# Optimization experiments

Measured on AMD Instinct MI355X. Metric: run time of the kernel, lower is better.

The kernel has to match this reference:

```python
import jax, jax.numpy as jnp
import numpy as np

USER_NUM = 100000
ITEM_NUM = 50000
EMBED_DIM = 64
N_LAYERS = 2
NNZ_UU, NNZ_UI, NNZ_II = 1600000, 2000000, 800000


def setup_inputs() -> dict:
    key = jax.random.key(0)
    ks = jax.random.split(key, 11)
    return {
        "user_embedding": jax.random.normal(ks[0], (USER_NUM, EMBED_DIM), jnp.float32),
        "item_embedding": jax.random.normal(ks[1], (ITEM_NUM, EMBED_DIM), jnp.float32),
        "uu_val": jax.random.uniform(ks[2], (NNZ_UU,), jnp.float32),
        "ui_val": jax.random.uniform(ks[3], (NNZ_UI,), jnp.float32),
        "ii_val": jax.random.uniform(ks[4], (NNZ_II,), jnp.float32),
        "uu_rows": jax.random.randint(ks[5], (NNZ_UU,), 0, USER_NUM, jnp.int32),
        "uu_cols": jax.random.randint(ks[6], (NNZ_UU,), 0, USER_NUM, jnp.int32),
        "ui_rows": jax.random.randint(ks[7], (NNZ_UI,), 0, USER_NUM, jnp.int32),
        "ui_cols": jax.random.randint(ks[8], (NNZ_UI,), 0, ITEM_NUM, jnp.int32),
        "ii_rows": jax.random.randint(ks[9], (NNZ_II,), 0, ITEM_NUM, jnp.int32),
        "ii_cols": jax.random.randint(ks[10], (NNZ_II,), 0, ITEM_NUM, jnp.int32),
    }


def _spmm(rows, cols, vals, x, n_out):
    # sparse(COO) @ dense: gather source features, scale by edge value, scatter-add to rows
    return jax.ops.segment_sum(vals[:, None] * x[cols], rows, num_segments=n_out)


def reference(user_embedding, item_embedding, uu_val, ui_val, ii_val,
              uu_rows, uu_cols, ui_rows, ui_cols, ii_rows, ii_cols):
    u = user_embedding
    i = item_embedding
    # running sum for mean over (n_layers + 1) layer outputs
    u_sum, i_sum = u, i
    for _ in range(N_LAYERS):
        u_from_i = _spmm(ui_rows, ui_cols, ui_val, i, USER_NUM)        # user_item_graph @ item
        i_from_u = _spmm(ui_cols, ui_rows, ui_val, u, ITEM_NUM)        # user_item_graph.T @ user
        uu = _spmm(uu_rows, uu_cols, uu_val, u, USER_NUM)              # user_graph @ user
        ii = _spmm(ii_rows, ii_cols, ii_val, i, ITEM_NUM)              # item_graph @ item
        u = 0.5 * (uu + u_from_i)   # mean over stacked pair
        i = 0.5 * (ii + i_from_u)
        u_sum = u_sum + u
        i_sum = i_sum + i
    inv = 1.0 / (N_LAYERS + 1)
    return u_sum * inv, i_sum * inv
```

## Files before the change

kernel.cpp:

```cpp
#include <hip/hip_runtime.h>

typedef _Float16 half8_t __attribute__((ext_vector_type(8)));
typedef _Float16 half4_t __attribute__((ext_vector_type(4)));

#define NU 100000
#define NI 50000
#define NR (NU + NI)
#define D 64
#define COARSE 1024
#define RPB 147
#define CAP 8800
#define CHUNK 6144
#define RPT 6
#define NT4 (NR * 16)
#define PKSLACK 448

__global__ void init_kernel(const float4* __restrict__ ue, const float4* __restrict__ ie,
                            float4* __restrict__ out, half4_t* __restrict__ curh) {
    int idx = blockIdx.x * 256 + threadIdx.x;
    if (idx >= NT4) return;
    float4 v = (idx < NU * 16) ? ue[idx] : ie[idx - NU * 16];
    out[idx] = v;
    half4_t h;
    h[0] = (_Float16)v.x; h[1] = (_Float16)v.y; h[2] = (_Float16)v.z; h[3] = (_Float16)v.w;
    curh[idx] = h;
}

__device__ __forceinline__ int place_dest(int p, const int* ui_r, const int* ui_c,
                                          const int* uu_r, const int* ii_r,
                                          int n_ui, int n_uu) {
    if (p < 2 * n_ui) {
        int e = p >> 1;
        return (p & 1) ? NU + ui_c[e] : ui_r[e];
    } else if (p < 2 * n_ui + n_uu) {
        return uu_r[p - 2 * n_ui];
    } else {
        return NU + ii_r[p - 2 * n_ui - n_uu];
    }
}

__global__ void count_kernel(const int* __restrict__ ui_r, const int* __restrict__ ui_c,
                             const int* __restrict__ uu_r, const int* __restrict__ ii_r,
                             int* __restrict__ m, int n_ui, int n_uu, int nnzt) {
    __shared__ int cnt[COARSE];
    int tid = threadIdx.x;
    cnt[tid] = 0;
    __syncthreads();
    int blk0 = blockIdx.x * CHUNK;
#pragma unroll
    for (int k = 0; k < RPT; k++) {
        int p = blk0 + k * 1024 + tid;
        if (p < nnzt) {
            int dest = place_dest(p, ui_r, ui_c, uu_r, ii_r, n_ui, n_uu);
            atomicAdd(&cnt[dest / RPB], 1);
        }
    }
    __syncthreads();
    m[blockIdx.x * COARSE + tid] = cnt[tid];
}

__global__ void colsum_kernel(const int* __restrict__ m, int* __restrict__ tots, int nblk) {
    __shared__ int s[256];
    int c = blockIdx.x, tid = threadIdx.x;
    int sum = 0;
    for (int b = tid; b < nblk; b += 256) sum += m[b * COARSE + c];
    s[tid] = sum;
    __syncthreads();
    for (int off = 128; off > 0; off >>= 1) {
        if (tid < off) s[tid] += s[tid + off];
        __syncthreads();
    }
    if (tid == 0) tots[c] = s[0];
}

__global__ void scan1_kernel(const int* __restrict__ tots, int* __restrict__ coarse_base) {
    __shared__ int s[COARSE];
    int tid = threadIdx.x;
    int x = tots[tid];
    s[tid] = x;
    __syncthreads();
    for (int off = 1; off < COARSE; off <<= 1) {
        int t = (tid >= off) ? s[tid - off] : 0;
        __syncthreads();
        s[tid] += t;
        __syncthreads();
    }
    coarse_base[tid] = s[tid] - x;
    if (tid == COARSE - 1) coarse_base[COARSE] = s[tid];
}

__global__ void rebase_kernel(int* __restrict__ m, const int* __restrict__ coarse_base, int nblk) {
    __shared__ int s[256];
    int c = blockIdx.x, tid = threadIdx.x;
    int K = (nblk + 255) / 256;
    int b0 = tid * K;
    int b1 = b0 + K;
    if (b1 > nblk) b1 = nblk;
    int sum = 0;
    for (int b = b0; b < b1; b++) sum += m[b * COARSE + c];
    s[tid] = sum;
    __syncthreads();
    for (int off = 1; off < 256; off <<= 1) {
        int t = (tid >= off) ? s[tid - off] : 0;
        __syncthreads();
        s[tid] += t;
        __syncthreads();
    }
    int run = coarse_base[c] + s[tid] - sum;
    for (int b = b0; b < b1; b++) {
        int v = m[b * COARSE + c];
        m[b * COARSE + c] = run;
        run += v;
    }
}

__global__ void place_kernel(const int* __restrict__ ui_r, const int* __restrict__ ui_c,
                             const float* __restrict__ ui_v,
                             const int* __restrict__ uu_r, const int* __restrict__ uu_c,
                             const float* __restrict__ uu_v,
                             const int* __restrict__ ii_r, const int* __restrict__ ii_c,
                             const float* __restrict__ ii_v,
                             const int* __restrict__ m, uint2* __restrict__ scratch,
                             int n_ui, int n_uu, int nnzt) {
    __shared__ uint2 rec[CHUNK];
    __shared__ int cnt[COARSE];
    __shared__ int lbase[COARSE];
    __shared__ int base_s[COARSE];
    __shared__ int s_ntot;
    int tid = threadIdx.x;
    cnt[tid] = 0;
    __syncthreads();
    int blk0 = blockIdx.x * CHUNK;
    int rk[RPT];
#pragma unroll
    for (int k = 0; k < RPT; k++) {
        int p = blk0 + k * 1024 + tid;
        rk[k] = -1;
        if (p < nnzt) {
            int dest = place_dest(p, ui_r, ui_c, uu_r, ii_r, n_ui, n_uu);
            int c = dest / RPB;
            int lr = atomicAdd(&cnt[c], 1);
            rk[k] = (c << 14) | lr;
        }
    }
    __syncthreads();
    int own = cnt[tid];
    lbase[tid] = own;
    __syncthreads();
    for (int off = 1; off < COARSE; off <<= 1) {
        int t = (tid >= off) ? lbase[tid - off] : 0;
        __syncthreads();
        lbase[tid] += t;
        __syncthreads();
    }
    int incl = lbase[tid];
    __syncthreads();
    lbase[tid] = incl - own;
    if (tid == COARSE - 1) s_ntot = incl;
    base_s[tid] = m[blockIdx.x * COARSE + tid];
    __syncthreads();
#pragma unroll
    for (int k = 0; k < RPT; k++) {
        int p = blk0 + k * 1024 + tid;
        if (p >= nnzt) continue;
        int dest, src;
        float v;
        if (p < 2 * n_ui) {
            int e = p >> 1;
            int r = ui_r[e], cc = ui_c[e];
            v = ui_v[e];
            if (p & 1) { dest = NU + cc; src = r; }
            else       { dest = r; src = NU + cc; }
        } else if (p < 2 * n_ui + n_uu) {
            int e = p - 2 * n_ui;
            dest = uu_r[e]; src = uu_c[e]; v = uu_v[e];
        } else {
            int e = p - 2 * n_ui - n_uu;
            dest = NU + ii_r[e]; src = NU + ii_c[e]; v = ii_v[e];
        }
        int c  = rk[k] >> 14;
        int lr = rk[k] & 0x3FFF;
        int dl = dest - c * RPB;
        _Float16 hv = (_Float16)v;
        unsigned short us;
        __builtin_memcpy(&us, &hv, 2);
        rec[lbase[c] + lr] = make_uint2(((unsigned)dl << 18) | (unsigned)src,
                                        ((unsigned)c << 16) | (unsigned)us);
    }
    __syncthreads();
    int ntot = s_ntot;
    for (int i = tid; i < ntot; i += 1024) {
        uint2 r = rec[i];
        int c = r.y >> 16;
        scratch[base_s[c] + (i - lbase[c])] = r;
    }
}

__global__ void csr_kernel(const uint2* __restrict__ scratch, const int* __restrict__ coarse_base,
                           int* __restrict__ ptr, int* __restrict__ pk_src,
                           unsigned short* __restrict__ pk_val) {
    __shared__ int s[1024];
    __shared__ int fine[256];
    __shared__ int fill[256];
    __shared__ int lsrc[CAP];
    __shared__ unsigned short lval[CAP];
    __shared__ int s_pn;
    int c = blockIdx.x, tid = threadIdx.x;
    int rbeg = c * RPB;
    int rcnt = NR - rbeg;
    if (rcnt > RPB) rcnt = RPB;
    if (rcnt < 0) rcnt = 0;
    int base = coarse_base[c], end = coarse_base[c + 1];
    int n = end - base;
    int pkc    = ((base + 3) & ~3) + c * PKSLACK;
    int pknext = ((end  + 3) & ~3) + (c + 1) * PKSLACK;
    if (tid < 256) fine[tid] = 0;
    __syncthreads();
    for (int i = tid; i < n; i += 1024)
        atomicAdd(&fine[scratch[base + i].x >> 18], 1);
    __syncthreads();
    int own = (tid < 256) ? fine[tid] : 0;
    int own4 = (own + 3) & ~3;
    s[tid] = own4;
    __syncthreads();
    for (int off = 1; off < 256; off <<= 1) {
        int t = (tid >= off) ? s[tid - off] : 0;
        __syncthreads();
        s[tid] += t;
        __syncthreads();
    }
    int excl4 = s[tid] - own4;
    if (tid < rcnt) ptr[rbeg + tid] = pkc + excl4;
    if (tid == 0 && rbeg + rcnt == NR) ptr[NR] = pknext;
    if (tid < 256) fill[tid] = excl4;
    if (tid == 255) s_pn = s[255];
    __syncthreads();
    int pn = s_pn;
    if (pn <= CAP) {
        for (int i = tid; i < pn; i += 1024) { lsrc[i] = 0; lval[i] = 0; }
        __syncthreads();
        for (int i = tid; i < n; i += 1024) {
            uint2 rec = scratch[base + i];
            int dl = rec.x >> 18;
            int slot = atomicAdd(&fill[dl], 1);
            lsrc[slot] = rec.x & 0x3FFFF;
            lval[slot] = (unsigned short)rec.y;
        }
        __syncthreads();
        for (int i = tid; i < pn; i += 1024) {
            pk_src[pkc + i] = lsrc[i] << 7;
            pk_val[pkc + i] = lval[i];
        }
        for (int i = pkc + pn + tid; i < pknext; i += 1024) { pk_src[i] = 0; pk_val[i] = 0; }
    } else {
        for (int i = pkc + tid; i < pknext; i += 1024) { pk_src[i] = 0; pk_val[i] = 0; }
        __syncthreads();
        for (int i = tid; i < n; i += 1024) {
            uint2 rec = scratch[base + i];
            int dl = rec.x >> 18;
            int slot = atomicAdd(&fill[dl], 1);
            pk_src[pkc + slot] = (rec.x & 0x3FFFF) << 7;
            pk_val[pkc + slot] = (unsigned short)rec.y;
        }
    }
}

__global__ void spmm_fused(const int* __restrict__ ptr, const int* __restrict__ pk_src,
                           const half4_t* __restrict__ pk_val4,
                           const half8_t* __restrict__ src,
                           half8_t* __restrict__ nexth, float4* __restrict__ out,
                           float final_scale, int store_next) {
    int w = (int)((blockIdx.x * blockDim.x + threadIdx.x) >> 6);
    int lane = threadIdx.x & 63;
    if (w >= NR) return;
    int g = lane >> 3;
    int fl = lane & 7;
    const char* sph = (const char*)src + (fl << 4);
    const int4* ps = (const int4*)pk_src;

    int b = ptr[w], e = ptr[w + 1];
    int q0 = b >> 2, qe = e >> 2;

    float acc[8];
#pragma unroll
    for (int k = 0; k < 8; k++) acc[k] = 0.f;

    for (int q = q0 + g; q < qe; q += 8) {
        int4 sa = ps[q];
        half4_t va = pk_val4[q];
        half8_t x0 = *(const half8_t*)(sph + sa.x);
        half8_t x1 = *(const half8_t*)(sph + sa.y);
        half8_t x2 = *(const half8_t*)(sph + sa.z);
        half8_t x3 = *(const half8_t*)(sph + sa.w);
        float v0 = (float)va[0];
        float v1 = (float)va[1];
        float v2 = (float)va[2];
        float v3 = (float)va[3];
#pragma unroll
        for (int k = 0; k < 8; k++) {
            acc[k] += v0 * (float)x0[k];
            acc[k] += v1 * (float)x1[k];
            acc[k] += v2 * (float)x2[k];
            acc[k] += v3 * (float)x3[k];
        }
    }

#pragma unroll
    for (int k = 0; k < 8; k++) {
        acc[k] += __shfl_xor(acc[k], 8);
        acc[k] += __shfl_xor(acc[k], 16);
        acc[k] += __shfl_xor(acc[k], 32);
    }

    if (lane < 8) {
        float h[8];
#pragma unroll
        for (int k = 0; k < 8; k++) h[k] = 0.5f * acc[k];
        if (store_next) {
            half8_t hh;
#pragma unroll
            for (int k = 0; k < 8; k++) hh[k] = (_Float16)h[k];
            nexth[w * 8 + lane] = hh;
        }
        float4* op = out + (size_t)w * 16 + lane * 2;
        float4 o0 = op[0];
        float4 o1 = op[1];
        o0.x = (o0.x + h[0]) * final_scale;
        o0.y = (o0.y + h[1]) * final_scale;
        o0.z = (o0.z + h[2]) * final_scale;
        o0.w = (o0.w + h[3]) * final_scale;
        o1.x = (o1.x + h[4]) * final_scale;
        o1.y = (o1.y + h[5]) * final_scale;
        o1.z = (o1.z + h[6]) * final_scale;
        o1.w = (o1.w + h[7]) * final_scale;
        op[0] = o0;
        op[1] = o1;
    }
}

extern "C" void kernel_launch(void* const* d_in, const int* in_sizes, int n_in,
                              void* d_out, int out_size, void* d_ws, size_t ws_size,
                              hipStream_t stream) {
    const float* ue      = (const float*)d_in[0];
    const float* ie      = (const float*)d_in[1];
    const float* uu_val  = (const float*)d_in[2];
    const float* ui_val  = (const float*)d_in[3];
    const float* ii_val  = (const float*)d_in[4];
    const int*   uu_rows = (const int*)d_in[5];
    const int*   uu_cols = (const int*)d_in[6];
    const int*   ui_rows = (const int*)d_in[7];
    const int*   ui_cols = (const int*)d_in[8];
    const int*   ii_rows = (const int*)d_in[9];
    const int*   ii_cols = (const int*)d_in[10];

    const int NNZ_UU = in_sizes[2];
    const int NNZ_UI = in_sizes[3];
    const int NNZ_II = in_sizes[4];
    const int NNZT   = 2 * NNZ_UI + NNZ_UU + NNZ_II;
    const int NBLK   = (NNZT + CHUNK - 1) / CHUNK;
    const int PKTOT  = NNZT + PKSLACK * COARSE + 64;

    float* out = (float*)d_out;

    char* wsb = (char*)d_ws;
    half8_t* curh   = (half8_t*)wsb;
    uint2*   scratch = (uint2*)(wsb + (size_t)NR * 128);
    half8_t* nexth  = (half8_t*)scratch;
    int*     pk_src = (int*)(scratch + NNZT);
    unsigned short* pk_val = (unsigned short*)(pk_src + PKTOT);
    int*     ptr    = (int*)(pk_val + PKTOT);
    int*     coarse_base = ptr + (NR + 1);
    int*     tots   = coarse_base + (COARSE + 1);
    int*     m      = tots + COARSE;

    init_kernel<<<(NT4 + 255) / 256, 256, 0, stream>>>(
        (const float4*)ue, (const float4*)ie, (float4*)out, (half4_t*)curh);

    count_kernel<<<NBLK, 1024, 0, stream>>>(
        ui_rows, ui_cols, uu_rows, ii_rows, m, NNZ_UI, NNZ_UU, NNZT);

    colsum_kernel<<<COARSE, 256, 0, stream>>>(m, tots, NBLK);
    scan1_kernel<<<1, 1024, 0, stream>>>(tots, coarse_base);
    rebase_kernel<<<COARSE, 256, 0, stream>>>(m, coarse_base, NBLK);

    place_kernel<<<NBLK, 1024, 0, stream>>>(
        ui_rows, ui_cols, ui_val, uu_rows, uu_cols, uu_val,
        ii_rows, ii_cols, ii_val, m, scratch, NNZ_UI, NNZ_UU, NNZT);

    csr_kernel<<<COARSE, 1024, 0, stream>>>(scratch, coarse_base, ptr, pk_src, pk_val);

    int blocks = (NR * 64 + 511) / 512;

    spmm_fused<<<blocks, 512, 0, stream>>>(
        ptr, pk_src, (const half4_t*)pk_val, curh, nexth, (float4*)out, 1.0f, 1);

    spmm_fused<<<blocks, 512, 0, stream>>>(
        ptr, pk_src, (const half4_t*)pk_val, nexth, curh, (float4*)out, 1.0f / 3.0f, 0);
}
```

Measured before the change: 491.7 us.

## Process four rows per wavefront in SpMM with two edge-groups per row

Changes the SpMM work mapping so that each 64-lane wavefront handles four output rows, each served by 16 lanes split into two edge groups, where before a whole wave handled one row with eight groups. The cross-lane reduction shrinks to a single shuffle, and the half-precision store and fp32 output update are split across the two halves. The aim is to cut idle lanes and reduction overhead, since the average row has about 29 edges (roughly 7 packed quads). In exchange, each lane runs a longer serial loop with less memory parallelism per row, and rows of different lengths within one wave can diverge.

```diff
diff --git a/kernel.cpp b/kernel.cpp
--- a/kernel.cpp
+++ b/kernel.cpp
@@ -270,22 +270,24 @@
                            const half8_t* __restrict__ src,
                            half8_t* __restrict__ nexth, float4* __restrict__ out,
                            float final_scale, int store_next) {
-    int w = (int)((blockIdx.x * blockDim.x + threadIdx.x) >> 6);
+    int wave = (int)((blockIdx.x * blockDim.x + threadIdx.x) >> 6);
     int lane = threadIdx.x & 63;
-    if (w >= NR) return;
-    int g = lane >> 3;
+    int sl = lane >> 4;
+    int h  = (lane >> 3) & 1;
     int fl = lane & 7;
+    int row = wave * 4 + sl;
+    if (row >= NR) return;
     const char* sph = (const char*)src + (fl << 4);
     const int4* ps = (const int4*)pk_src;
 
-    int b = ptr[w], e = ptr[w + 1];
+    int b = ptr[row], e = ptr[row + 1];
     int q0 = b >> 2, qe = e >> 2;
 
     float acc[8];
 #pragma unroll
     for (int k = 0; k < 8; k++) acc[k] = 0.f;
 
-    for (int q = q0 + g; q < qe; q += 8) {
+    for (int q = q0 + h; q < qe; q += 2) {
         int4 sa = ps[q];
         half4_t va = pk_val4[q];
         half8_t x0 = *(const half8_t*)(sph + sa.x);
@@ -306,33 +308,31 @@
     }
 
 #pragma unroll
-    for (int k = 0; k < 8; k++) {
-        acc[k] += __shfl_xor(acc[k], 8);
-        acc[k] += __shfl_xor(acc[k], 16);
-        acc[k] += __shfl_xor(acc[k], 32);
-    }
-
-    if (lane < 8) {
-        float h[8];
-#pragma unroll
-        for (int k = 0; k < 8; k++) h[k] = 0.5f * acc[k];
+    for (int k = 0; k < 8; k++) acc[k] += __shfl_xor(acc[k], 8);
+
+    float hv[8];
+#pragma unroll
+    for (int k = 0; k < 8; k++) hv[k] = 0.5f * acc[k];
+
+    if (h == 0) {
         if (store_next) {
             half8_t hh;
 #pragma unroll
-            for (int k = 0; k < 8; k++) hh[k] = (_Float16)h[k];
-            nexth[w * 8 + lane] = hh;
-        }
-        float4* op = out + (size_t)w * 16 + lane * 2;
+            for (int k = 0; k < 8; k++) hh[k] = (_Float16)hv[k];
+            nexth[row * 8 + fl] = hh;
+        }
+    } else {
+        float4* op = out + (size_t)row * 16 + fl * 2;
         float4 o0 = op[0];
         float4 o1 = op[1];
-        o0.x = (o0.x + h[0]) * final_scale;
-        o0.y = (o0.y + h[1]) * final_scale;
-        o0.z = (o0.z + h[2]) * final_scale;
-        o0.w = (o0.w + h[3]) * final_scale;
-        o1.x = (o1.x + h[4]) * final_scale;
-        o1.y = (o1.y + h[5]) * final_scale;
-        o1.z = (o1.z + h[6]) * final_scale;
-        o1.w = (o1.w + h[7]) * final_scale;
+        o0.x = (o0.x + hv[0]) * final_scale;
+        o0.y = (o0.y + hv[1]) * final_scale;
+        o0.z = (o0.z + hv[2]) * final_scale;
+        o0.w = (o0.w + hv[3]) * final_scale;
+        o1.x = (o1.x + hv[4]) * final_scale;
+        o1.y = (o1.y + hv[5]) * final_scale;
+        o1.z = (o1.z + hv[6]) * final_scale;
+        o1.w = (o1.w + hv[7]) * final_scale;
         op[0] = o0;
         op[1] = o1;
     }
@@ -389,7 +389,8 @@
 
     csr_kernel<<<COARSE, 1024, 0, stream>>>(scratch, coarse_base, ptr, pk_src, pk_val);
 
-    int blocks = (NR * 64 + 511) / 512;
+    int waves = (NR + 3) / 4;
+    int blocks = (waves * 64 + 511) / 512;
 
     spmm_fused<<<blocks, 512, 0, stream>>>(
         ptr, pk_src, (const half4_t*)pk_val, curh, nexth, (float4*)out, 1.0f, 1);
```

Result: slower. 507.4 us (+3.2%).

## Replace per-block count matrix with global atomics; drop colsum and rebase kernels

Applied to the files above, without the earlier changes.

Count blocks now atomically add their bucket counts into a global totals array, and place blocks claim output ranges with atomicAdd on a per-bucket cursor. This removes the colsum and rebase kernel launches and the per-block count matrix traffic. The place kernel keeps each edge's source and value in registers so it does not reload the inputs. The csr kernel caches scratch records in registers, and init no longer writes the float output: layer 0 writes it directly and layer 1 adds the original embeddings. Record order within a bucket becomes nondeterministic, which can change float summation order between runs.

```diff
diff --git a/kernel.cpp b/kernel.cpp
--- a/kernel.cpp
+++ b/kernel.cpp
@@ -12,15 +12,16 @@
 #define CAP 8800
 #define CHUNK 6144
 #define RPT 6
+#define RPT2 9
 #define NT4 (NR * 16)
 #define PKSLACK 448
 
 __global__ void init_kernel(const float4* __restrict__ ue, const float4* __restrict__ ie,
-                            float4* __restrict__ out, half4_t* __restrict__ curh) {
+                            half4_t* __restrict__ curh, int* __restrict__ tots) {
     int idx = blockIdx.x * 256 + threadIdx.x;
+    if (idx < COARSE) tots[idx] = 0;
     if (idx >= NT4) return;
     float4 v = (idx < NU * 16) ? ue[idx] : ie[idx - NU * 16];
-    out[idx] = v;
     half4_t h;
     h[0] = (_Float16)v.x; h[1] = (_Float16)v.y; h[2] = (_Float16)v.z; h[3] = (_Float16)v.w;
     curh[idx] = h;
@@ -41,7 +42,7 @@
 
 __global__ void count_kernel(const int* __restrict__ ui_r, const int* __restrict__ ui_c,
                              const int* __restrict__ uu_r, const int* __restrict__ ii_r,
-                             int* __restrict__ m, int n_ui, int n_uu, int nnzt) {
+                             int* __restrict__ tots, int n_ui, int n_uu, int nnzt) {
     __shared__ int cnt[COARSE];
     int tid = threadIdx.x;
     cnt[tid] = 0;
@@ -56,24 +57,11 @@
         }
     }
     __syncthreads();
-    m[blockIdx.x * COARSE + tid] = cnt[tid];
-}
-
-__global__ void colsum_kernel(const int* __restrict__ m, int* __restrict__ tots, int nblk) {
-    __shared__ int s[256];
-    int c = blockIdx.x, tid = threadIdx.x;
-    int sum = 0;
-    for (int b = tid; b < nblk; b += 256) sum += m[b * COARSE + c];
-    s[tid] = sum;
-    __syncthreads();
-    for (int off = 128; off > 0; off >>= 1) {
-        if (tid < off) s[tid] += s[tid + off];
-        __syncthreads();
-    }
-    if (tid == 0) tots[c] = s[0];
-}
-
-__global__ void scan1_kernel(const int* __restrict__ tots, int* __restrict__ coarse_base) {
+    if (cnt[tid]) atomicAdd(&tots[tid], cnt[tid]);
+}
+
+__global__ void scan1_kernel(const int* __restrict__ tots, int* __restrict__ coarse_base,
+                             int* __restrict__ cursor) {
     __shared__ int s[COARSE];
     int tid = threadIdx.x;
     int x = tots[tid];
@@ -85,33 +73,10 @@
         s[tid] += t;
         __syncthreads();
     }
-    coarse_base[tid] = s[tid] - x;
+    int excl = s[tid] - x;
+    coarse_base[tid] = excl;
+    cursor[tid] = excl;
     if (tid == COARSE - 1) coarse_base[COARSE] = s[tid];
-}
-
-__global__ void rebase_kernel(int* __restrict__ m, const int* __restrict__ coarse_base, int nblk) {
-    __shared__ int s[256];
-    int c = blockIdx.x, tid = threadIdx.x;
-    int K = (nblk + 255) / 256;
-    int b0 = tid * K;
-    int b1 = b0 + K;
-    if (b1 > nblk) b1 = nblk;
-    int sum = 0;
-    for (int b = b0; b < b1; b++) sum += m[b * COARSE + c];
-    s[tid] = sum;
-    __syncthreads();
-    for (int off = 1; off < 256; off <<= 1) {
-        int t = (tid >= off) ? s[tid - off] : 0;
-        __syncthreads();
-        s[tid] += t;
-        __syncthreads();
-    }
-    int run = coarse_base[c] + s[tid] - sum;
-    for (int b = b0; b < b1; b++) {
-        int v = m[b * COARSE + c];
-        m[b * COARSE + c] = run;
-        run += v;
-    }
 }
 
 __global__ void place_kernel(const int* __restrict__ ui_r, const int* __restrict__ ui_c,
@@ -120,7 +85,7 @@
                              const float* __restrict__ uu_v,
                              const int* __restrict__ ii_r, const int* __restrict__ ii_c,
                              const float* __restrict__ ii_v,
-                             const int* __restrict__ m, uint2* __restrict__ scratch,
+                             int* __restrict__ cursor, uint2* __restrict__ scratch,
                              int n_ui, int n_uu, int nnzt) {
     __shared__ uint2 rec[CHUNK];
     __shared__ int cnt[COARSE];
@@ -131,20 +96,41 @@
     cnt[tid] = 0;
     __syncthreads();
     int blk0 = blockIdx.x * CHUNK;
-    int rk[RPT];
+    unsigned rk[RPT];
+    int sk[RPT];
+    unsigned short vk[RPT];
 #pragma unroll
     for (int k = 0; k < RPT; k++) {
         int p = blk0 + k * 1024 + tid;
-        rk[k] = -1;
+        rk[k] = 0xFFFFFFFFu;
         if (p < nnzt) {
-            int dest = place_dest(p, ui_r, ui_c, uu_r, ii_r, n_ui, n_uu);
+            int dest, src;
+            float v;
+            if (p < 2 * n_ui) {
+                int e = p >> 1;
+                int r = ui_r[e], cc = ui_c[e];
+                v = ui_v[e];
+                if (p & 1) { dest = NU + cc; src = r; }
+                else       { dest = r; src = NU + cc; }
+            } else if (p < 2 * n_ui + n_uu) {
+                int e = p - 2 * n_ui;
+                dest = uu_r[e]; src = uu_c[e]; v = uu_v[e];
+            } else {
+                int e = p - 2 * n_ui - n_uu;
+                dest = NU + ii_r[e]; src = NU + ii_c[e]; v = ii_v[e];
+            }
             int c = dest / RPB;
             int lr = atomicAdd(&cnt[c], 1);
-            rk[k] = (c << 14) | lr;
+            int dl = dest - c * RPB;
+            rk[k] = ((unsigned)dl << 24) | ((unsigned)c << 14) | (unsigned)lr;
+            sk[k] = src;
+            _Float16 hv = (_Float16)v;
+            __builtin_memcpy(&vk[k], &hv, 2);
         }
     }
     __syncthreads();
     int own = cnt[tid];
+    if (own) base_s[tid] = atomicAdd(&cursor[tid], own);
     lbase[tid] = own;
     __syncthreads();
     for (int off = 1; off < COARSE; off <<= 1) {
@@ -157,35 +143,15 @@
     __syncthreads();
     lbase[tid] = incl - own;
     if (tid == COARSE - 1) s_ntot = incl;
-    base_s[tid] = m[blockIdx.x * COARSE + tid];
     __syncthreads();
 #pragma unroll
     for (int k = 0; k < RPT; k++) {
-        int p = blk0 + k * 1024 + tid;
-        if (p >= nnzt) continue;
-        int dest, src;
-        float v;
-        if (p < 2 * n_ui) {
-            int e = p >> 1;
-            int r = ui_r[e], cc = ui_c[e];
-            v = ui_v[e];
-            if (p & 1) { dest = NU + cc; src = r; }
-            else       { dest = r; src = NU + cc; }
-        } else if (p < 2 * n_ui + n_uu) {
-            int e = p - 2 * n_ui;
-            dest = uu_r[e]; src = uu_c[e]; v = uu_v[e];
-        } else {
-            int e = p - 2 * n_ui - n_uu;
-            dest = NU + ii_r[e]; src = NU + ii_c[e]; v = ii_v[e];
-        }
-        int c  = rk[k] >> 14;
+        if (rk[k] == 0xFFFFFFFFu) continue;
+        int c  = (rk[k] >> 14) & 0x3FF;
         int lr = rk[k] & 0x3FFF;
-        int dl = dest - c * RPB;
-        _Float16 hv = (_Float16)v;
-        unsigned short us;
-        __builtin_memcpy(&us, &hv, 2);
-        rec[lbase[c] + lr] = make_uint2(((unsigned)dl << 18) | (unsigned)src,
-                                        ((unsigned)c << 16) | (unsigned)us);
+        int dl = rk[k] >> 24;
+        rec[lbase[c] + lr] = make_uint2(((unsigned)dl << 18) | (unsigned)sk[k],
+                                        ((unsigned)c << 16) | (unsigned)vk[k]);
     }
     __syncthreads();
     int ntot = s_ntot;
@@ -214,10 +180,23 @@
     int n = end - base;
     int pkc    = ((base + 3) & ~3) + c * PKSLACK;
     int pknext = ((end  + 3) & ~3) + (c + 1) * PKSLACK;
+    bool small = (n <= RPT2 * 1024);
     if (tid < 256) fine[tid] = 0;
     __syncthreads();
-    for (int i = tid; i < n; i += 1024)
-        atomicAdd(&fine[scratch[base + i].x >> 18], 1);
+    uint2 rc[RPT2];
+    if (small) {
+#pragma unroll
+        for (int k = 0; k < RPT2; k++) {
+            int i = k * 1024 + tid;
+            if (i < n) {
+                rc[k] = scratch[base + i];
+                atomicAdd(&fine[rc[k].x >> 18], 1);
+            }
+        }
+    } else {
+        for (int i = tid; i < n; i += 1024)
+            atomicAdd(&fine[scratch[base + i].x >> 18], 1);
+    }
     __syncthreads();
     int own = (tid < 256) ? fine[tid] : 0;
     int own4 = (own + 3) & ~3;
@@ -236,15 +215,18 @@
     if (tid == 255) s_pn = s[255];
     __syncthreads();
     int pn = s_pn;
-    if (pn <= CAP) {
+    if (small && pn <= CAP) {
         for (int i = tid; i < pn; i += 1024) { lsrc[i] = 0; lval[i] = 0; }
         __syncthreads();
-        for (int i = tid; i < n; i += 1024) {
-            uint2 rec = scratch[base + i];
-            int dl = rec.x >> 18;
-            int slot = atomicAdd(&fill[dl], 1);
-            lsrc[slot] = rec.x & 0x3FFFF;
-            lval[slot] = (unsigned short)rec.y;
+#pragma unroll
+        for (int k = 0; k < RPT2; k++) {
+            int i = k * 1024 + tid;
+            if (i < n) {
+                int dl = rc[k].x >> 18;
+                int slot = atomicAdd(&fill[dl], 1);
+                lsrc[slot] = rc[k].x & 0x3FFFF;
+                lval[slot] = (unsigned short)rc[k].y;
+            }
         }
         __syncthreads();
         for (int i = tid; i < pn; i += 1024) {
@@ -256,11 +238,11 @@
         for (int i = pkc + tid; i < pknext; i += 1024) { pk_src[i] = 0; pk_val[i] = 0; }
         __syncthreads();
         for (int i = tid; i < n; i += 1024) {
-            uint2 rec = scratch[base + i];
-            int dl = rec.x >> 18;
+            uint2 r2 = scratch[base + i];
+            int dl = r2.x >> 18;
             int slot = atomicAdd(&fill[dl], 1);
-            pk_src[pkc + slot] = (rec.x & 0x3FFFF) << 7;
-            pk_val[pkc + slot] = (unsigned short)rec.y;
+            pk_src[pkc + slot] = (r2.x & 0x3FFFF) << 7;
+            pk_val[pkc + slot] = (unsigned short)r2.y;
         }
     }
 }
@@ -269,7 +251,8 @@
                            const half4_t* __restrict__ pk_val4,
                            const half8_t* __restrict__ src,
                            half8_t* __restrict__ nexth, float4* __restrict__ out,
-                           float final_scale, int store_next) {
+                           const float4* __restrict__ ue4, const float4* __restrict__ ie4,
+                           int layer) {
     int w = (int)((blockIdx.x * blockDim.x + threadIdx.x) >> 6);
     int lane = threadIdx.x & 63;
     if (w >= NR) return;
@@ -316,25 +299,31 @@
         float h[8];
 #pragma unroll
         for (int k = 0; k < 8; k++) h[k] = 0.5f * acc[k];
-        if (store_next) {
+        float4* op = out + (size_t)w * 16 + lane * 2;
+        if (layer == 0) {
             half8_t hh;
 #pragma unroll
             for (int k = 0; k < 8; k++) hh[k] = (_Float16)h[k];
             nexth[w * 8 + lane] = hh;
-        }
-        float4* op = out + (size_t)w * 16 + lane * 2;
-        float4 o0 = op[0];
-        float4 o1 = op[1];
-        o0.x = (o0.x + h[0]) * final_scale;
-        o0.y = (o0.y + h[1]) * final_scale;
-        o0.z = (o0.z + h[2]) * final_scale;
-        o0.w = (o0.w + h[3]) * final_scale;
-        o1.x = (o1.x + h[4]) * final_scale;
-        o1.y = (o1.y + h[5]) * final_scale;
-        o1.z = (o1.z + h[6]) * final_scale;
-        o1.w = (o1.w + h[7]) * final_scale;
-        op[0] = o0;
-        op[1] = o1;
+            op[0] = make_float4(h[0], h[1], h[2], h[3]);
+            op[1] = make_float4(h[4], h[5], h[6], h[7]);
+        } else {
+            const float4* ep = (w < NU) ? (ue4 + (size_t)w * 16 + lane * 2)
+                                        : (ie4 + (size_t)(w - NU) * 16 + lane * 2);
+            const float inv3 = 1.0f / 3.0f;
+            float4 o0 = op[0], o1 = op[1];
+            float4 e0 = ep[0], e1 = ep[1];
+            o0.x = ((o0.x + e0.x) + h[0]) * inv3;
+            o0.y = ((o0.y + e0.y) + h[1]) * inv3;
+            o0.z = ((o0.z + e0.z) + h[2]) * inv3;
+            o0.w = ((o0.w + e0.w) + h[3]) * inv3;
+            o1.x = ((o1.x + e1.x) + h[4]) * inv3;
+            o1.y = ((o1.y + e1.y) + h[5]) * inv3;
+            o1.z = ((o1.z + e1.z) + h[6]) * inv3;
+            o1.w = ((o1.w + e1.w) + h[7]) * inv3;
+            op[0] = o0;
+            op[1] = o1;
+        }
     }
 }
 
@@ -371,29 +360,29 @@
     int*     ptr    = (int*)(pk_val + PKTOT);
     int*     coarse_base = ptr + (NR + 1);
     int*     tots   = coarse_base + (COARSE + 1);
-    int*     m      = tots + COARSE;
+    int*     cursor = tots + COARSE;
 
     init_kernel<<<(NT4 + 255) / 256, 256, 0, stream>>>(
-        (const float4*)ue, (const float4*)ie, (float4*)out, (half4_t*)curh);
+        (const float4*)ue, (const float4*)ie, (half4_t*)curh, tots);
 
     count_kernel<<<NBLK, 1024, 0, stream>>>(
-        ui_rows, ui_cols, uu_rows, ii_rows, m, NNZ_UI, NNZ_UU, NNZT);
-
-    colsum_kernel<<<COARSE, 256, 0, stream>>>(m, tots, NBLK);
-    scan1_kernel<<<1, 1024, 0, stream>>>(tots, coarse_base);
-    rebase_kernel<<<COARSE, 256, 0, stream>>>(m, coarse_base, NBLK);
+        ui_rows, ui_cols, uu_rows, ii_rows, tots, NNZ_UI, NNZ_UU, NNZT);
+
+    scan1_kernel<<<1, 1024, 0, stream>>>(tots, coarse_base, cursor);
 
     place_kernel<<<NBLK, 1024, 0, stream>>>(
         ui_rows, ui_cols, ui_val, uu_rows, uu_cols, uu_val,
-        ii_rows, ii_cols, ii_val, m, scratch, NNZ_UI, NNZ_UU, NNZT);
+        ii_rows, ii_cols, ii_val, cursor, scratch, NNZ_UI, NNZ_UU, NNZT);
 
     csr_kernel<<<COARSE, 1024, 0, stream>>>(scratch, coarse_base, ptr, pk_src, pk_val);
 
     int blocks = (NR * 64 + 511) / 512;
 
     spmm_fused<<<blocks, 512, 0, stream>>>(
-        ptr, pk_src, (const half4_t*)pk_val, curh, nexth, (float4*)out, 1.0f, 1);
+        ptr, pk_src, (const half4_t*)pk_val, curh, nexth, (float4*)out,
+        (const float4*)ue, (const float4*)ie, 0);
 
     spmm_fused<<<blocks, 512, 0, stream>>>(
-        ptr, pk_src, (const half4_t*)pk_val, nexth, curh, (float4*)out, 1.0f / 3.0f, 0);
-}
+        ptr, pk_src, (const half4_t*)pk_val, nexth, curh, (float4*)out,
+        (const float4*)ue, (const float4*)ie, 1);
+}
```

After: 472.1 us. -4.0%, faster.
